# Kernel tuning notes

Hardware: AMD Instinct MI355X
Metric: run time of the kernel (lower is better)

## Reference

```python
import jax, jax.numpy as jnp
from jax import lax
import numpy as np

INPUT_SIZE = 1
HIDDEN_SIZE = 32
BATCH = 256
SEQ_LEN = 2048


def setup_inputs() -> dict:
    key = jax.random.key(0)
    kx, k1, k2, k3, k4 = jax.random.split(key, 5)
    H, I = HIDDEN_SIZE, INPUT_SIZE
    s = 1.0 / np.sqrt(H)  # torch LSTM default init: U(-1/sqrt(H), 1/sqrt(H))
    x = jax.random.normal(kx, (BATCH, SEQ_LEN, I), dtype=jnp.float32)
    W_ih = jax.random.uniform(k1, (4 * H, I), minval=-s, maxval=s, dtype=jnp.float32)
    W_hh = jax.random.uniform(k2, (4 * H, H), minval=-s, maxval=s, dtype=jnp.float32)
    b_ih = jax.random.uniform(k3, (4 * H,), minval=-s, maxval=s, dtype=jnp.float32)
    b_hh = jax.random.uniform(k4, (4 * H,), minval=-s, maxval=s, dtype=jnp.float32)
    return {"x": x, "W_ih": W_ih, "W_hh": W_hh, "b_ih": b_ih, "b_hh": b_hh}


def _lstm_last_hidden(x, W_ih, W_hh, b_ih, b_hh):
    # x: [B, T, I] (batch_first). PyTorch gate order: i, f, g, o.
    B = x.shape[0]
    H = W_hh.shape[1]
    # Precompute input contribution for all timesteps in one GEMM: [B, T, 4H]
    xg = jnp.einsum('bti,gi->btg', x, W_ih) + (b_ih + b_hh)
    xg = jnp.transpose(xg, (1, 0, 2))  # [T, B, 4H] for scan over time

    h0 = jnp.zeros((B, H), dtype=x.dtype)
    c0 = jnp.zeros((B, H), dtype=x.dtype)

    def step(carry, gx):
        h, c = carry
        gates = gx + h @ W_hh.T  # [B, 4H]
        i, f, g, o = jnp.split(gates, 4, axis=-1)
        i = jax.nn.sigmoid(i)
        f = jax.nn.sigmoid(f)
        g = jnp.tanh(g)
        o = jax.nn.sigmoid(o)
        c = f * c + i * g
        h = o * jnp.tanh(c)
        return (h, c), None

    (h_last, _c_last), _ = lax.scan(step, (h0, c0), xg)
    return h_last  # [B, H] == hidden[0] in the torch module


def reference(x, W_ih, W_hh, b_ih, b_hh):
    return _lstm_last_hidden(x, W_ih, W_hh, b_ih, b_hh)
```

## Files before the change

### kernel.cpp

```cpp
#include <hip/hip_runtime.h>

#define HSZ 32
#define TSEQ 2048
#define NBATCH 256

typedef float v2f __attribute__((ext_vector_type(2)));
typedef unsigned int v2u __attribute__((ext_vector_type(2)));

__device__ __forceinline__ v2f make2(float a, float b) {
    v2f r; r.x = a; r.y = b; return r;
}

__device__ __forceinline__ float hw_exp2(float x) {
#if __has_builtin(__builtin_amdgcn_exp2f)
    return __builtin_amdgcn_exp2f(x);
#else
    return exp2f(x);
#endif
}

__device__ __forceinline__ float hw_rcp(float x) {
#if __has_builtin(__builtin_amdgcn_rcpf)
    return __builtin_amdgcn_rcpf(x);
#else
    return 1.0f / x;
#endif
}

__device__ __forceinline__ float readlane_f(float v, int lane) {
    return __uint_as_float(__builtin_amdgcn_readlane(__float_as_uint(v), lane));
}

__device__ __forceinline__ float half_sum(float v) {
#if __has_builtin(__builtin_amdgcn_permlane32_swap)
    v2u r = __builtin_amdgcn_permlane32_swap(__float_as_uint(v), __float_as_uint(v), false, false);
    return __uint_as_float(r.x) + __uint_as_float(r.y);
#else
    return v + __shfl_xor(v, 32, 64);
#endif
}

#if __has_builtin(__builtin_elementwise_fma)
#define PKFMA(a, b, cc) __builtin_elementwise_fma((a), (b), (cc))
#else
__device__ __forceinline__ v2f PKFMA(v2f a, v2f b, v2f c) {
    return make2(fmaf(a.x, b.x, c.x), fmaf(a.y, b.y, c.y));
}
#endif

#define NL2E -1.44269504088896340736f

__global__ __launch_bounds__(64, 1) void lstm_last_kernel(
    const float* __restrict__ x,
    const float* __restrict__ W_ih,
    const float* __restrict__ W_hh,
    const float* __restrict__ b_ih,
    const float* __restrict__ b_hh,
    float* __restrict__ out)
{
    const int b    = blockIdx.x;
    const int l    = threadIdx.x;
    const int k    = l & 31;
    const int half = l >> 5;
    const int row0 = l;
    const int row1 = l + 64;

    __shared__ float x_lds[TSEQ + 4];

    const float4* xrow4 = (const float4*)(x + (size_t)b * TSEQ);
    float4* xl4 = (float4*)x_lds;
    #pragma unroll
    for (int j = 0; j < (TSEQ / 4) / 64; ++j)
        xl4[j * 64 + l] = xrow4[j * 64 + l];
    if (l == 0) x_lds[TSEQ] = 0.0f;

    const float sc0 = NL2E;
    const float sc1 = half ? NL2E : 2.0f * NL2E;

    v2f wp0[HSZ/2], wp1[HSZ/2];
    #pragma unroll
    for (int j = 0; j < HSZ; j += 4) {
        float4 a  = *(const float4*)(W_hh + row0 * HSZ + j);
        float4 c4 = *(const float4*)(W_hh + row1 * HSZ + j);
        wp0[j/2]     = make2(a.x * sc0,  a.y * sc0);
        wp0[j/2 + 1] = make2(a.z * sc0,  a.w * sc0);
        wp1[j/2]     = make2(c4.x * sc1, c4.y * sc1);
        wp1[j/2 + 1] = make2(c4.z * sc1, c4.w * sc1);
    }
    const float wx0   = W_ih[row0] * sc0;
    const float wx1   = W_ih[row1] * sc1;
    const float bias0 = (b_ih[row0] + b_hh[row0]) * sc0;
    const float bias1 = (b_ih[row1] + b_hh[row1]) * sc1;

    const float s1mul = half ? 1.0f : 2.0f;
    const float s1add = half ? 0.0f : -1.0f;

    float c  = 0.0f;
    float hk = 0.0f;

    __syncthreads();
    float xt = x_lds[0];

    #pragma unroll 1
    for (int t = 0; t < TSEQ; ++t) {
        v2f hp[HSZ/2];
        #pragma unroll
        for (int m = 0; m < HSZ/2; ++m) {
            hp[m].x = readlane_f(hk, 32 + 2*m);
            hp[m].y = readlane_f(hk, 32 + 2*m + 1);
        }

        float xt_next = x_lds[t + 1];

        v2f q0 = make2(fmaf(wx0, xt, bias0), 0.f);
        v2f q1 = make2(0.f, 0.f), q2 = make2(0.f, 0.f), q3 = make2(0.f, 0.f);
        #pragma unroll
        for (int m = 0; m < HSZ/2; m += 4) {
            q0 = PKFMA(wp0[m],   hp[m],   q0);
            q1 = PKFMA(wp0[m+1], hp[m+1], q1);
            q2 = PKFMA(wp0[m+2], hp[m+2], q2);
            q3 = PKFMA(wp0[m+3], hp[m+3], q3);
        }
        v2f r0 = (q0 + q1) + (q2 + q3);
        float d0 = r0.x + r0.y;
        float a0 = hw_rcp(1.0f + hw_exp2(d0));

        v2f u0 = make2(fmaf(wx1, xt, bias1), 0.f);
        v2f u1 = make2(0.f, 0.f), u2 = make2(0.f, 0.f), u3 = make2(0.f, 0.f);
        #pragma unroll
        for (int m = 0; m < HSZ/2; m += 4) {
            u0 = PKFMA(wp1[m],   hp[m],   u0);
            u1 = PKFMA(wp1[m+1], hp[m+1], u1);
            u2 = PKFMA(wp1[m+2], hp[m+2], u2);
            u3 = PKFMA(wp1[m+3], hp[m+3], u3);
        }
        v2f r1 = (u0 + u1) + (u2 + u3);
        float d1 = r1.x + r1.y;
        float a1 = fmaf(s1mul, hw_rcp(1.0f + hw_exp2(d1)), s1add);

        float v  = a0 * (half ? c : a1);
        float cn = half_sum(v);
        c = cn;

        float th = fmaf(2.0f, hw_rcp(1.0f + hw_exp2(cn * (2.0f * NL2E))), -1.0f);
        hk = a1 * th;

        xt = xt_next;
    }

    if (half) out[b * HSZ + k] = hk;
}

extern "C" void kernel_launch(void* const* d_in, const int* in_sizes, int n_in,
                              void* d_out, int out_size, void* d_ws, size_t ws_size,
                              hipStream_t stream) {
    const float* x    = (const float*)d_in[0];
    const float* W_ih = (const float*)d_in[1];
    const float* W_hh = (const float*)d_in[2];
    const float* b_ih = (const float*)d_in[3];
    const float* b_hh = (const float*)d_in[4];
    float* out = (float*)d_out;

    lstm_last_kernel<<<NBATCH, 64, 0, stream>>>(x, W_ih, W_hh, b_ih, b_hh, out);
}
```

Measured before the change: 423.9 us.

## Broadcast hidden state through LDS instead of per-lane readlane

Replaces the 32 scalar readlane broadcasts of h each step with a write of h to a small LDS buffer and vectorized float4 reads by all lanes. It also folds the tanh scaling constants into the cell-state gate (storing c pre-scaled by -2*log2e), so the tanh becomes one fused multiply-add, and it interleaves the two gate dot-products. The LDS write and read within a wave rely on implicit wave-level ordering with no barrier, which adds LDS latency to the recurrence critical path in place of the SALU readlane chain.

```diff
diff --git a/kernel.cpp b/kernel.cpp
--- a/kernel.cpp
+++ b/kernel.cpp
@@ -25,10 +25,6 @@
 #else
     return 1.0f / x;
 #endif
-}
-
-__device__ __forceinline__ float readlane_f(float v, int lane) {
-    return __uint_as_float(__builtin_amdgcn_readlane(__float_as_uint(v), lane));
 }
 
 __device__ __forceinline__ float half_sum(float v) {
@@ -66,6 +62,7 @@
     const int row1 = l + 64;
 
     __shared__ float x_lds[TSEQ + 4];
+    __shared__ float h_lds[64];
 
     const float4* xrow4 = (const float4*)(x + (size_t)b * TSEQ);
     float4* xl4 = (float4*)x_lds;
@@ -73,6 +70,7 @@
     for (int j = 0; j < (TSEQ / 4) / 64; ++j)
         xl4[j * 64 + l] = xrow4[j * 64 + l];
     if (l == 0) x_lds[TSEQ] = 0.0f;
+    h_lds[l] = 0.0f;
 
     const float sc0 = NL2E;
     const float sc1 = half ? NL2E : 2.0f * NL2E;
@@ -87,16 +85,18 @@
         wp1[j/2]     = make2(c4.x * sc1, c4.y * sc1);
         wp1[j/2 + 1] = make2(c4.z * sc1, c4.w * sc1);
     }
-    const float wx0   = W_ih[row0] * sc0;
-    const float wx1   = W_ih[row1] * sc1;
-    const float bias0 = (b_ih[row0] + b_hh[row0]) * sc0;
-    const float bias1 = (b_ih[row1] + b_hh[row1]) * sc1;
+    const v2f wxp0   = make2(W_ih[row0] * sc0, 0.0f);
+    const v2f wxp1   = make2(W_ih[row1] * sc1, 0.0f);
+    const v2f biasp0 = make2((b_ih[row0] + b_hh[row0]) * sc0, 0.0f);
+    const v2f biasp1 = make2((b_ih[row1] + b_hh[row1]) * sc1, 0.0f);
 
-    const float s1mul = half ? 1.0f : 2.0f;
-    const float s1add = half ? 0.0f : -1.0f;
+    const float s1mul = half ? 1.0f : -4.0f * NL2E;
+    const float s1add = half ? 0.0f :  2.0f * NL2E;
 
-    float c  = 0.0f;
+    float cc = 0.0f;
     float hk = 0.0f;
+
+    const int waddr = l ^ 32;
 
     __syncthreads();
     float xt = x_lds[0];
@@ -105,45 +105,48 @@
     for (int t = 0; t < TSEQ; ++t) {
         v2f hp[HSZ/2];
         #pragma unroll
-        for (int m = 0; m < HSZ/2; ++m) {
-            hp[m].x = readlane_f(hk, 32 + 2*m);
-            hp[m].y = readlane_f(hk, 32 + 2*m + 1);
+        for (int m = 0; m < 8; ++m) {
+            float4 v4 = ((const float4*)h_lds)[m];
+            hp[2*m]   = make2(v4.x, v4.y);
+            hp[2*m+1] = make2(v4.z, v4.w);
         }
 
         float xt_next = x_lds[t + 1];
 
-        v2f q0 = make2(fmaf(wx0, xt, bias0), 0.f);
+        v2f xtp = make2(xt, xt);
+
+        v2f q0 = PKFMA(wxp0, xtp, biasp0);
         v2f q1 = make2(0.f, 0.f), q2 = make2(0.f, 0.f), q3 = make2(0.f, 0.f);
+        v2f u0 = PKFMA(wxp1, xtp, biasp1);
+        v2f u1 = make2(0.f, 0.f), u2 = make2(0.f, 0.f), u3 = make2(0.f, 0.f);
         #pragma unroll
         for (int m = 0; m < HSZ/2; m += 4) {
             q0 = PKFMA(wp0[m],   hp[m],   q0);
             q1 = PKFMA(wp0[m+1], hp[m+1], q1);
             q2 = PKFMA(wp0[m+2], hp[m+2], q2);
             q3 = PKFMA(wp0[m+3], hp[m+3], q3);
-        }
-        v2f r0 = (q0 + q1) + (q2 + q3);
-        float d0 = r0.x + r0.y;
-        float a0 = hw_rcp(1.0f + hw_exp2(d0));
-
-        v2f u0 = make2(fmaf(wx1, xt, bias1), 0.f);
-        v2f u1 = make2(0.f, 0.f), u2 = make2(0.f, 0.f), u3 = make2(0.f, 0.f);
-        #pragma unroll
-        for (int m = 0; m < HSZ/2; m += 4) {
             u0 = PKFMA(wp1[m],   hp[m],   u0);
             u1 = PKFMA(wp1[m+1], hp[m+1], u1);
             u2 = PKFMA(wp1[m+2], hp[m+2], u2);
             u3 = PKFMA(wp1[m+3], hp[m+3], u3);
         }
+        v2f r0 = (q0 + q1) + (q2 + q3);
         v2f r1 = (u0 + u1) + (u2 + u3);
+        float d0 = r0.x + r0.y;
         float d1 = r1.x + r1.y;
+
+        float a0 = hw_rcp(1.0f + hw_exp2(d0));
         float a1 = fmaf(s1mul, hw_rcp(1.0f + hw_exp2(d1)), s1add);
+        float m2a1 = -2.0f * a1;
 
-        float v  = a0 * (half ? c : a1);
+        float v  = a0 * (half ? cc : a1);
         float cn = half_sum(v);
-        c = cn;
+        cc = cn;
 
-        float th = fmaf(2.0f, hw_rcp(1.0f + hw_exp2(cn * (2.0f * NL2E))), -1.0f);
-        hk = a1 * th;
+        float r = hw_rcp(1.0f + hw_exp2(cn));
+        hk = fmaf(m2a1, r, a1);
+
+        h_lds[waddr] = hk;
 
         xt = xt_next;
     }
```

After: 384.7 us (median of 2 runs). 9.2% less time.
